# Optimization experiments

Hardware: AMD Instinct MI355X
Metric: run time of the kernel (lower is better)

Reference implementation:

```python
import jax, jax.numpy as jnp
import numpy as np

B, S, D, H = 2, 2048, 1024, 16
DH = D // H
CAUSAL = True


def setup_inputs() -> dict:
    key = jax.random.key(0)
    ks = jax.random.split(key, 11)
    s = 1.0 / np.sqrt(D)
    return {
        "x": jax.random.normal(ks[0], (B, S, D), dtype=jnp.float32),
        "Wq": jax.random.uniform(ks[1], (D, D), jnp.float32, -s, s),
        "bq": jax.random.uniform(ks[2], (D,), jnp.float32, -s, s),
        "Wk": jax.random.uniform(ks[3], (D, D), jnp.float32, -s, s),
        "bk": jax.random.uniform(ks[4], (D,), jnp.float32, -s, s),
        "Wv": jax.random.uniform(ks[5], (D, D), jnp.float32, -s, s),
        "bv": jax.random.uniform(ks[6], (D,), jnp.float32, -s, s),
        "Wo": jax.random.uniform(ks[7], (D, D), jnp.float32, -s, s),
        "bo": jax.random.uniform(ks[8], (D,), jnp.float32, -s, s),
        "ln_g": jnp.ones((D,), jnp.float32),
        "ln_b": jnp.zeros((D,), jnp.float32),
    }


def reference(x, Wq, bq, Wk, bk, Wv, bv, Wo, bo, ln_g, ln_b):
    scale = np.sqrt(DH).astype(np.float32)
    # projections -> [B, H, S, DH]
    def proj(W, b):
        return (x @ W.T + b).reshape(B, S, H, DH).transpose(0, 2, 1, 3)
    Q, K, V = proj(Wq, bq), proj(Wk, bk), proj(Wv, bv)
    scores = jnp.einsum("bhsd,bhtd->bhst", Q, K) / scale  # [B,H,S,S]
    if CAUSAL:
        causal = jnp.tril(jnp.ones((S, S), dtype=bool))
        scores = jnp.where(causal, scores, -jnp.inf)
    attn = jax.nn.softmax(scores, axis=-1)
    ctx = jnp.einsum("bhst,bhtd->bhsd", attn, V)
    ctx = ctx.transpose(0, 2, 1, 3).reshape(B, S, D)
    attn_out = ctx @ Wo.T + bo
    y = x + attn_out
    mu = jnp.mean(y, axis=-1, keepdims=True)
    var = jnp.mean(jnp.square(y - mu), axis=-1, keepdims=True)
    return (y - mu) / jnp.sqrt(var + 1e-5) * ln_g + ln_b
```

## Files before the change

### kernel.cpp

```cpp
#include <hip/hip_runtime.h>
#include <stdint.h>

#define B_   2
#define S_   2048
#define D_   1024
#define H_   16
#define DH_  64
#define MTOK (B_*S_)

typedef __attribute__((ext_vector_type(8))) short  short8v;
typedef __attribute__((ext_vector_type(4))) float  f32x4;
typedef __attribute__((ext_vector_type(16))) float f32x16;
typedef __attribute__((ext_vector_type(4))) unsigned int uint4v;

__device__ __forceinline__ unsigned short f2bf(float f) {
  unsigned int u = __builtin_bit_cast(unsigned int, f);
  unsigned int r = (u + 0x7fffu + ((u >> 16) & 1u)) >> 16;
  return (unsigned short)r;
}

__device__ __forceinline__ f32x4 zero4() { f32x4 v = {0.f, 0.f, 0.f, 0.f}; return v; }
__device__ __forceinline__ f32x16 zero16() {
  f32x16 v;
#pragma unroll
  for (int i = 0; i < 16; ++i) v[i] = 0.f;
  return v;
}

__device__ __forceinline__ unsigned int cvtpk(float lo, float hi) {
  unsigned int d;
  asm("v_cvt_pk_bf16_f32 %0, %1, %2" : "=v"(d) : "v"(lo), "v"(hi));
  return d;
}
__device__ __forceinline__ void plswap(unsigned int& a, unsigned int& b) {
  asm("v_permlane32_swap_b32 %0, %1" : "+v"(a), "+v"(b));
}

__device__ __forceinline__ void gload16(const void* g, void* l) {
  __builtin_amdgcn_global_load_lds(
      (const __attribute__((address_space(1))) void*)g,
      (__attribute__((address_space(3))) void*)l, 16, 0, 0);
}

__global__ void cvt_kernel(const float* __restrict__ in, unsigned short* __restrict__ out, int n4) {
  int i = blockIdx.x * blockDim.x + threadIdx.x;
  if (i >= n4) return;
  float4 v = reinterpret_cast<const float4*>(in)[i];
  ushort4 o;
  o.x = f2bf(v.x); o.y = f2bf(v.y); o.z = f2bf(v.z); o.w = f2bf(v.w);
  reinterpret_cast<ushort4*>(out)[i] = o;
}

__global__ void cvt4_kernel(const float* __restrict__ w0, const float* __restrict__ w1,
                            const float* __restrict__ w2, const float* __restrict__ w3,
                            unsigned short* __restrict__ o0, unsigned short* __restrict__ o1,
                            unsigned short* __restrict__ o2, unsigned short* __restrict__ o3,
                            int n4) {
  int i = blockIdx.x * blockDim.x + threadIdx.x;
  if (i >= n4) return;
  const float* in = (blockIdx.y == 0) ? w0 : (blockIdx.y == 1) ? w1 : (blockIdx.y == 2) ? w2 : w3;
  unsigned short* out = (blockIdx.y == 0) ? o0 : (blockIdx.y == 1) ? o1 : (blockIdx.y == 2) ? o2 : o3;
  float4 v = reinterpret_cast<const float4*>(in)[i];
  ushort4 o;
  o.x = f2bf(v.x); o.y = f2bf(v.y); o.z = f2bf(v.z); o.w = f2bf(v.w);
  reinterpret_cast<ushort4*>(out)[i] = o;
}

__device__ __forceinline__ void gemm_mainloop(
    const unsigned short* __restrict__ A, const unsigned short* __restrict__ Bt,
    int K, int m0, int n0, unsigned short* As, unsigned short* Bs, f32x4 acc[4][4])
{
  const int tid = threadIdx.x;
  const int lane = tid & 63, wid = tid >> 6;
  const int wr = wid >> 1, wc = wid & 1;
  const int l15 = lane & 15, g = lane >> 4;

#pragma unroll
  for (int mi = 0; mi < 4; ++mi)
#pragma unroll
    for (int ni = 0; ni < 4; ++ni) acc[mi][ni] = zero4();

  const int nk = K >> 6;
  for (int k0i = 0; k0i < nk; ++k0i) {
    const int k0 = k0i << 6;
    __syncthreads();
#pragma unroll
    for (int it = 0; it < 4; ++it) {
      int fa = it * 256 + tid;
      int row = fa >> 3, slot = fa & 7;
      int gs = slot ^ (row & 7);
      gload16(A + (size_t)(m0 + row) * K + k0 + gs * 8, (char*)As + fa * 16);
    }
#pragma unroll
    for (int it = 0; it < 4; ++it) {
      int fa = it * 256 + tid;
      int row = fa >> 3, slot = fa & 7;
      int gs = slot ^ (row & 7);
      gload16(Bt + (size_t)(n0 + row) * K + k0 + gs * 8, (char*)Bs + fa * 16);
    }
    __syncthreads();
#pragma unroll
    for (int kk = 0; kk < 2; ++kk) {
      short8v af[4], bfr[4];
#pragma unroll
      for (int mi = 0; mi < 4; ++mi) {
        int row = wr * 64 + mi * 16 + l15;
        int slot = (kk * 4 + g) ^ (row & 7);
        af[mi] = *(const short8v*)((const char*)As + row * 128 + slot * 16);
      }
#pragma unroll
      for (int ni = 0; ni < 4; ++ni) {
        int row = wc * 64 + ni * 16 + l15;
        int slot = (kk * 4 + g) ^ (row & 7);
        bfr[ni] = *(const short8v*)((const char*)Bs + row * 128 + slot * 16);
      }
#pragma unroll
      for (int mi = 0; mi < 4; ++mi)
#pragma unroll
        for (int ni = 0; ni < 4; ++ni)
          acc[mi][ni] = __builtin_amdgcn_mfma_f32_16x16x32_bf16(af[mi], bfr[ni], acc[mi][ni], 0, 0, 0);
    }
  }
}

__global__ __launch_bounds__(256) void gemm_qkv_kernel(
    const unsigned short* __restrict__ xb,
    const unsigned short* __restrict__ wqb, const unsigned short* __restrict__ wkb,
    const unsigned short* __restrict__ wvb,
    const float* __restrict__ bq, const float* __restrict__ bk, const float* __restrict__ bv,
    unsigned short* __restrict__ Qb, unsigned short* __restrict__ Kb, unsigned short* __restrict__ VTb)
{
  __shared__ __align__(16) unsigned short As[128 * 64];
  __shared__ __align__(16) unsigned short Bs[128 * 64];
  const int z = blockIdx.z;
  const unsigned short* Bt = (z == 0) ? wqb : (z == 1) ? wkb : wvb;
  const float* bias = (z == 0) ? bq : (z == 1) ? bk : bv;
  const float scl = (z == 0) ? 0.180336880f : 1.0f;
  const int m0 = blockIdx.y * 128, n0 = blockIdx.x * 128;

  f32x4 acc[4][4];
  gemm_mainloop(xb, Bt, D_, m0, n0, As, Bs, acc);

  const int tid = threadIdx.x, lane = tid & 63, wid = tid >> 6;
  const int wr = wid >> 1, wc = wid & 1, l15 = lane & 15, g = lane >> 4;
#pragma unroll
  for (int ni = 0; ni < 4; ++ni) {
    int n = n0 + wc * 64 + ni * 16 + l15;
    float bia = bias[n];
    int hh = n >> 6, dh = n & 63;
#pragma unroll
    for (int mi = 0; mi < 4; ++mi) {
      int mbase = m0 + wr * 64 + mi * 16 + 4 * g;
      int b = mbase >> 11;
      int s0 = mbase & 2047;
      if (z < 2) {
        unsigned short* o = (z == 0) ? Qb : Kb;
#pragma unroll
        for (int r = 0; r < 4; ++r) {
          float v = (acc[mi][ni][r] + bia) * scl;
          o[(((size_t)(b * H_ + hh) * S_ + (s0 + r)) << 6) + dh] = f2bf(v);
        }
      } else {
        ushort4 o;
        o.x = f2bf(acc[mi][ni][0] + bia);
        o.y = f2bf(acc[mi][ni][1] + bia);
        o.z = f2bf(acc[mi][ni][2] + bia);
        o.w = f2bf(acc[mi][ni][3] + bia);
        *(ushort4*)(VTb + ((size_t)(b * H_ + hh) * DH_ + dh) * S_ + s0) = o;
      }
    }
  }
}

__device__ __forceinline__ void stage_tile128(
    const unsigned short* Kh, const unsigned short* Vh, int t0, char* base, int tid)
{
#pragma unroll
  for (int it = 0; it < 4; ++it) {
    int fa = it * 256 + tid;
    int row = fa >> 3, slot = fa & 7, gs = slot ^ (row & 7);
    gload16(Kh + (size_t)(t0 + row) * DH_ + gs * 8, base + fa * 16);
  }
#pragma unroll
  for (int it = 0; it < 4; ++it) {
    int fa = it * 256 + tid;
    int row = fa >> 4, slot = fa & 15;
    int gs = slot ^ (row & 7);
    gload16(Vh + (size_t)row * S_ + t0 + gs * 8, base + 16384 + fa * 16);
  }
}

__global__ __launch_bounds__(256, 2) void attn_kernel(
    const unsigned short* __restrict__ Qb, const unsigned short* __restrict__ Kb,
    const unsigned short* __restrict__ VTb, unsigned short* __restrict__ ctxb)
{
  __shared__ __align__(16) char smem[65536];
  const int tid = threadIdx.x, lane = tid & 63, wid = tid >> 6;
  const int l31 = lane & 31, h = lane >> 5;
  const int fid = blockIdx.x;
  const int bh = (fid & 7) * 4 + ((fid >> 3) & 3);
  const int qpos = fid >> 5;
  const int qi = (qpos < 8) ? qpos : 23 - qpos;
  const int qblk = qi * 128;
  const int q0w = qblk + wid * 32;
  const int qg = q0w + l31;
  const unsigned short* Qh = Qb + (size_t)bh * S_ * DH_;
  const unsigned short* Kh = Kb + (size_t)bh * S_ * DH_;
  const unsigned short* Vh = VTb + (size_t)bh * DH_ * S_;

  short8v qf[4];
#pragma unroll
  for (int kk = 0; kk < 4; ++kk)
    qf[kk] = *(const short8v*)(Qh + (size_t)qg * DH_ + kk * 16 + h * 8);

  f32x16 ctx0 = zero16(), ctx1 = zero16();
  float mrun = -3e38f, lrun = 0.f;

  const int ntm1 = qi;
  stage_tile128(Kh, Vh, 0, smem, tid);
  asm volatile("s_waitcnt vmcnt(0)" ::: "memory");
  __builtin_amdgcn_s_barrier();
  asm volatile("" ::: "memory");

  for (int t = 0; t <= ntm1; ++t) {
    if (t < ntm1) stage_tile128(Kh, Vh, (t + 1) << 7, smem + (((t + 1) & 1) * 32768), tid);
    const char* Kbuf = smem + (t & 1) * 32768;
    const char* Vbuf = Kbuf + 16384;
#pragma unroll
    for (int sub = 0; sub < 2; ++sub) {
      const int t0 = (t << 7) + (sub << 6);
      if (t0 <= q0w + 31) {
        const char* Kt = Kbuf + sub * 8192;

        f32x16 s0 = zero16(), s1 = zero16();
        __builtin_amdgcn_s_setprio(1);
#pragma unroll
        for (int kk = 0; kk < 4; ++kk) {
          int slot = (2 * kk + h) ^ (l31 & 7);
          short8v kf0 = *(const short8v*)(Kt + l31 * 128 + slot * 16);
          short8v kf1 = *(const short8v*)(Kt + (32 + l31) * 128 + slot * 16);
          s0 = __builtin_amdgcn_mfma_f32_32x32x16_bf16(kf0, qf[kk], s0, 0, 0, 0);
          s1 = __builtin_amdgcn_mfma_f32_32x32x16_bf16(kf1, qf[kk], s1, 0, 0, 0);
        }
        __builtin_amdgcn_s_setprio(0);
        if (t0 + 63 > q0w) {
#pragma unroll
          for (int r = 0; r < 16; ++r) {
            int k0i = (r & 3) + 8 * (r >> 2) + 4 * h;
            if (t0 + k0i > qg) s0[r] = -1e30f;
            if (t0 + k0i + 32 > qg) s1[r] = -1e30f;
          }
        }
        float tm;
        {
          float m01[8];
#pragma unroll
          for (int r = 0; r < 8; ++r)
            m01[r] = fmaxf(fmaxf(s0[r], s0[r + 8]), fmaxf(s1[r], s1[r + 8]));
          float a = fmaxf(fmaxf(m01[0], m01[1]), fmaxf(m01[2], m01[3]));
          float b = fmaxf(fmaxf(m01[4], m01[5]), fmaxf(m01[6], m01[7]));
          tm = fmaxf(a, b);
        }
        tm = fmaxf(tm, __shfl_xor(tm, 32));

        if (!__all(tm <= mrun + 8.f)) {
          float mnew = fmaxf(mrun, tm);
          float al = exp2f(mrun - mnew);
#pragma unroll
          for (int r = 0; r < 16; ++r) { ctx0[r] *= al; ctx1[r] *= al; }
          lrun *= al;
          mrun = mnew;
        }
        float p[32];
        float psa0 = 0.f, psa1 = 0.f, psa2 = 0.f, psa3 = 0.f;
#pragma unroll
        for (int r = 0; r < 16; r += 4) {
          p[r + 0] = exp2f(s0[r + 0] - mrun); psa0 += p[r + 0];
          p[r + 1] = exp2f(s0[r + 1] - mrun); psa1 += p[r + 1];
          p[r + 2] = exp2f(s0[r + 2] - mrun); psa2 += p[r + 2];
          p[r + 3] = exp2f(s0[r + 3] - mrun); psa3 += p[r + 3];
        }
#pragma unroll
        for (int r = 0; r < 16; r += 4) {
          p[16 + r + 0] = exp2f(s1[r + 0] - mrun); psa0 += p[16 + r + 0];
          p[16 + r + 1] = exp2f(s1[r + 1] - mrun); psa1 += p[16 + r + 1];
          p[16 + r + 2] = exp2f(s1[r + 2] - mrun); psa2 += p[16 + r + 2];
          p[16 + r + 3] = exp2f(s1[r + 3] - mrun); psa3 += p[16 + r + 3];
        }
        float ps = (psa0 + psa1) + (psa2 + psa3);
        ps += __shfl_xor(ps, 32);
        lrun += ps;

        unsigned int pk[16];
#pragma unroll
        for (int m = 0; m < 16; ++m) pk[m] = cvtpk(p[2 * m], p[2 * m + 1]);
#pragma unroll
        for (int base = 0; base < 16; base += 4) {
          plswap(pk[base + 0], pk[base + 2]);
          plswap(pk[base + 1], pk[base + 3]);
        }
        __builtin_amdgcn_s_setprio(1);
#pragma unroll
        for (int dt = 0; dt < 2; ++dt) {
          int row = dt * 32 + l31;
#pragma unroll
          for (int kt = 0; kt < 4; ++kt) {
            int slot = (2 * kt + h) ^ (row & 7);
            short8v vf = *(const short8v*)(Vbuf + row * 256 + sub * 128 + slot * 16);
            uint4v u = {pk[4 * kt], pk[4 * kt + 1], pk[4 * kt + 2], pk[4 * kt + 3]};
            short8v pf = __builtin_bit_cast(short8v, u);
            if (dt == 0) ctx0 = __builtin_amdgcn_mfma_f32_32x32x16_bf16(vf, pf, ctx0, 0, 0, 0);
            else         ctx1 = __builtin_amdgcn_mfma_f32_32x32x16_bf16(vf, pf, ctx1, 0, 0, 0);
          }
        }
        __builtin_amdgcn_s_setprio(0);
      }
    }
    asm volatile("s_waitcnt vmcnt(0)" ::: "memory");
    __builtin_amdgcn_s_barrier();
    asm volatile("" ::: "memory");
  }

  float cf[32];
#pragma unroll
  for (int r = 0; r < 16; ++r) { cf[r] = ctx0[r]; cf[16 + r] = ctx1[r]; }
  const int b = bh >> 4, hcol = (bh & 15) * 64;
  unsigned short* orow = ctxb + (((size_t)(b * S_ + qg)) << 10) + hcol;
  float invL = 1.0f / lrun;
#pragma unroll
  for (int j = 0; j < 8; ++j) {
    uint2 w;
    w.x = cvtpk(cf[4 * j + 0] * invL, cf[4 * j + 1] * invL);
    w.y = cvtpk(cf[4 * j + 2] * invL, cf[4 * j + 3] * invL);
    *(uint2*)(orow + 32 * (j >> 2) + 8 * (j & 3) + 4 * h) = w;
  }
}

__global__ __launch_bounds__(256) void gemm_out_kernel(
    const unsigned short* __restrict__ ctxb, const unsigned short* __restrict__ wob,
    const float* __restrict__ bo, const float* __restrict__ x, float* __restrict__ y)
{
  __shared__ __align__(16) unsigned short As[128 * 64];
  __shared__ __align__(16) unsigned short Bs[128 * 64];
  const int m0 = blockIdx.y * 128, n0 = blockIdx.x * 128;
  f32x4 acc[4][4];
  gemm_mainloop(ctxb, wob, D_, m0, n0, As, Bs, acc);

  const int tid = threadIdx.x, lane = tid & 63, wid = tid >> 6;
  const int wr = wid >> 1, wc = wid & 1, l15 = lane & 15, g = lane >> 4;
#pragma unroll
  for (int ni = 0; ni < 4; ++ni) {
    int n = n0 + wc * 64 + ni * 16 + l15;
    float bia = bo[n];
#pragma unroll
    for (int mi = 0; mi < 4; ++mi) {
      int mbase = m0 + wr * 64 + mi * 16 + 4 * g;
#pragma unroll
      for (int r = 0; r < 4; ++r) {
        size_t idx = ((size_t)(mbase + r) << 10) + n;
        y[idx] = acc[mi][ni][r] + bia + x[idx];
      }
    }
  }
}

__global__ __launch_bounds__(256) void ln_kernel(
    float* __restrict__ y, const float* __restrict__ gw, const float* __restrict__ bw)
{
  const int row = blockIdx.x;
  float* p = y + ((size_t)row << 10);
  const int t = threadIdx.x;
  float4 v = *(const float4*)(p + t * 4);
  float s  = v.x + v.y + v.z + v.w;
  float s2 = v.x * v.x + v.y * v.y + v.z * v.z + v.w * v.w;
#pragma unroll
  for (int d = 1; d < 64; d <<= 1) { s += __shfl_xor(s, d); s2 += __shfl_xor(s2, d); }
  __shared__ float ps[4], ps2[4];
  const int lane = t & 63, wid = t >> 6;
  if (lane == 0) { ps[wid] = s; ps2[wid] = s2; }
  __syncthreads();
  s  = ps[0] + ps[1] + ps[2] + ps[3];
  s2 = ps2[0] + ps2[1] + ps2[2] + ps2[3];
  float mu  = s * (1.f / 1024.f);
  float var = s2 * (1.f / 1024.f) - mu * mu;
  float rstd = rsqrtf(var + 1e-5f);
  float4 gv = *(const float4*)(gw + t * 4);
  float4 bv = *(const float4*)(bw + t * 4);
  float4 o;
  o.x = (v.x - mu) * rstd * gv.x + bv.x;
  o.y = (v.y - mu) * rstd * gv.y + bv.y;
  o.z = (v.z - mu) * rstd * gv.z + bv.z;
  o.w = (v.w - mu) * rstd * gv.w + bv.w;
  *(float4*)(p + t * 4) = o;
}

extern "C" void kernel_launch(void* const* d_in, const int* in_sizes, int n_in,
                              void* d_out, int out_size, void* d_ws, size_t ws_size,
                              hipStream_t stream) {
  const float* x   = (const float*)d_in[0];
  const float* Wq  = (const float*)d_in[1];
  const float* bq  = (const float*)d_in[2];
  const float* Wk  = (const float*)d_in[3];
  const float* bk  = (const float*)d_in[4];
  const float* Wv  = (const float*)d_in[5];
  const float* bv  = (const float*)d_in[6];
  const float* Wo  = (const float*)d_in[7];
  const float* bo  = (const float*)d_in[8];
  const float* lng = (const float*)d_in[9];
  const float* lnb = (const float*)d_in[10];
  float* out = (float*)d_out;

  char* ws = (char*)d_ws;
  unsigned short* xb  = (unsigned short*)ws;                 ws += (size_t)MTOK * D_ * 2;
  unsigned short* wqb = (unsigned short*)ws;                 ws += (size_t)D_ * D_ * 2;
  unsigned short* wkb = (unsigned short*)ws;                 ws += (size_t)D_ * D_ * 2;
  unsigned short* wvb = (unsigned short*)ws;                 ws += (size_t)D_ * D_ * 2;
  unsigned short* wob = (unsigned short*)ws;                 ws += (size_t)D_ * D_ * 2;
  unsigned short* Qb  = (unsigned short*)ws;                 ws += (size_t)B_ * H_ * S_ * DH_ * 2;
  unsigned short* Kb  = (unsigned short*)ws;                 ws += (size_t)B_ * H_ * S_ * DH_ * 2;
  unsigned short* VTb = (unsigned short*)ws;                 ws += (size_t)B_ * H_ * DH_ * S_ * 2;
  unsigned short* ctxb = (unsigned short*)ws;                ws += (size_t)MTOK * D_ * 2;

  cvt_kernel<<<(MTOK * D_ / 4 + 255) / 256, 256, 0, stream>>>(x, xb, MTOK * D_ / 4);
  cvt4_kernel<<<dim3((D_ * D_ / 4 + 255) / 256, 4), 256, 0, stream>>>(
      Wq, Wk, Wv, Wo, wqb, wkb, wvb, wob, D_ * D_ / 4);

  gemm_qkv_kernel<<<dim3(D_ / 128, MTOK / 128, 3), 256, 0, stream>>>(
      xb, wqb, wkb, wvb, bq, bk, bv, Qb, Kb, VTb);

  attn_kernel<<<dim3((S_ / 128) * B_ * H_), 256, 0, stream>>>(Qb, Kb, VTb, ctxb);

  gemm_out_kernel<<<dim3(D_ / 128, MTOK / 128), 256, 0, stream>>>(ctxb, wob, bo, x, out);

  ln_kernel<<<MTOK, 256, 0, stream>>>(out, lng, lnb);
}
```

Measured before the change: 144.0 us.

## Double-buffer LDS tiles in GEMM mainloop to overlap loads with MFMA

```diff
diff --git a/kernel.cpp b/kernel.cpp
--- a/kernel.cpp
+++ b/kernel.cpp
@@ -66,6 +66,26 @@
   reinterpret_cast<ushort4*>(out)[i] = o;
 }
 
+__device__ __forceinline__ void stage_gemm(
+    const unsigned short* __restrict__ A, const unsigned short* __restrict__ Bt,
+    int K, int m0, int n0, int k0, unsigned short* As, unsigned short* Bs, int tid)
+{
+#pragma unroll
+  for (int it = 0; it < 4; ++it) {
+    int fa = it * 256 + tid;
+    int row = fa >> 3, slot = fa & 7;
+    int gs = slot ^ (row & 7);
+    gload16(A + (size_t)(m0 + row) * K + k0 + gs * 8, (char*)As + fa * 16);
+  }
+#pragma unroll
+  for (int it = 0; it < 4; ++it) {
+    int fa = it * 256 + tid;
+    int row = fa >> 3, slot = fa & 7;
+    int gs = slot ^ (row & 7);
+    gload16(Bt + (size_t)(n0 + row) * K + k0 + gs * 8, (char*)Bs + fa * 16);
+  }
+}
+
 __device__ __forceinline__ void gemm_mainloop(
     const unsigned short* __restrict__ A, const unsigned short* __restrict__ Bt,
     int K, int m0, int n0, unsigned short* As, unsigned short* Bs, f32x4 acc[4][4])
@@ -81,24 +101,17 @@
     for (int ni = 0; ni < 4; ++ni) acc[mi][ni] = zero4();
 
   const int nk = K >> 6;
+  stage_gemm(A, Bt, K, m0, n0, 0, As, Bs, tid);
+  asm volatile("s_waitcnt vmcnt(0)" ::: "memory");
+  __builtin_amdgcn_s_barrier();
+  asm volatile("" ::: "memory");
+
   for (int k0i = 0; k0i < nk; ++k0i) {
-    const int k0 = k0i << 6;
-    __syncthreads();
-#pragma unroll
-    for (int it = 0; it < 4; ++it) {
-      int fa = it * 256 + tid;
-      int row = fa >> 3, slot = fa & 7;
-      int gs = slot ^ (row & 7);
-      gload16(A + (size_t)(m0 + row) * K + k0 + gs * 8, (char*)As + fa * 16);
-    }
-#pragma unroll
-    for (int it = 0; it < 4; ++it) {
-      int fa = it * 256 + tid;
-      int row = fa >> 3, slot = fa & 7;
-      int gs = slot ^ (row & 7);
-      gload16(Bt + (size_t)(n0 + row) * K + k0 + gs * 8, (char*)Bs + fa * 16);
-    }
-    __syncthreads();
+    if (k0i + 1 < nk)
+      stage_gemm(A, Bt, K, m0, n0, (k0i + 1) << 6,
+                 As + ((k0i + 1) & 1) * 8192, Bs + ((k0i + 1) & 1) * 8192, tid);
+    const unsigned short* Ab = As + (k0i & 1) * 8192;
+    const unsigned short* Bb = Bs + (k0i & 1) * 8192;
 #pragma unroll
     for (int kk = 0; kk < 2; ++kk) {
       short8v af[4], bfr[4];
@@ -106,13 +119,13 @@
       for (int mi = 0; mi < 4; ++mi) {
         int row = wr * 64 + mi * 16 + l15;
         int slot = (kk * 4 + g) ^ (row & 7);
-        af[mi] = *(const short8v*)((const char*)As + row * 128 + slot * 16);
+        af[mi] = *(const short8v*)((const char*)Ab + row * 128 + slot * 16);
       }
 #pragma unroll
       for (int ni = 0; ni < 4; ++ni) {
         int row = wc * 64 + ni * 16 + l15;
         int slot = (kk * 4 + g) ^ (row & 7);
-        bfr[ni] = *(const short8v*)((const char*)Bs + row * 128 + slot * 16);
+        bfr[ni] = *(const short8v*)((const char*)Bb + row * 128 + slot * 16);
       }
 #pragma unroll
       for (int mi = 0; mi < 4; ++mi)
@@ -120,6 +133,9 @@
         for (int ni = 0; ni < 4; ++ni)
           acc[mi][ni] = __builtin_amdgcn_mfma_f32_16x16x32_bf16(af[mi], bfr[ni], acc[mi][ni], 0, 0, 0);
     }
+    asm volatile("s_waitcnt vmcnt(0)" ::: "memory");
+    __builtin_amdgcn_s_barrier();
+    asm volatile("" ::: "memory");
   }
 }
 
@@ -130,8 +146,8 @@
     const float* __restrict__ bq, const float* __restrict__ bk, const float* __restrict__ bv,
     unsigned short* __restrict__ Qb, unsigned short* __restrict__ Kb, unsigned short* __restrict__ VTb)
 {
-  __shared__ __align__(16) unsigned short As[128 * 64];
-  __shared__ __align__(16) unsigned short Bs[128 * 64];
+  __shared__ __align__(16) unsigned short As[2 * 128 * 64];
+  __shared__ __align__(16) unsigned short Bs[2 * 128 * 64];
   const int z = blockIdx.z;
   const unsigned short* Bt = (z == 0) ? wqb : (z == 1) ? wkb : wvb;
   const float* bias = (z == 0) ? bq : (z == 1) ? bk : bv;
@@ -340,8 +356,8 @@
     const unsigned short* __restrict__ ctxb, const unsigned short* __restrict__ wob,
     const float* __restrict__ bo, const float* __restrict__ x, float* __restrict__ y)
 {
-  __shared__ __align__(16) unsigned short As[128 * 64];
-  __shared__ __align__(16) unsigned short Bs[128 * 64];
+  __shared__ __align__(16) unsigned short As[2 * 128 * 64];
+  __shared__ __align__(16) unsigned short Bs[2 * 128 * 64];
   const int m0 = blockIdx.y * 128, n0 = blockIdx.x * 128;
   f32x4 acc[4][4];
   gemm_mainloop(ctxb, wob, D_, m0, n0, As, Bs, acc);
```

Measured after the change: 155.9 us. 1.08x slower.
